# Performance work log

Hardware: AMD Instinct MI355X
Metric: run time of the kernel (lower is better)

## Reference

```python
import jax, jax.numpy as jnp
import numpy as np

N_NODES = 100000
N_EDGES = 1_600_000
N_ROIS = 400
HIDDEN = 128
N_GRAPHS = 512
OUT = 2


def setup_inputs() -> dict:
    key = jax.random.key(0)
    ks = jax.random.split(key, 7)
    x = jax.random.normal(ks[0], (N_NODES, N_ROIS), dtype=jnp.float32)
    edge_index = jax.random.randint(ks[1], (2, N_EDGES), 0, N_NODES, dtype=jnp.int32)
    # sorted graph-assignment vector; prepend arange so every graph id is non-empty
    rnd = jax.random.randint(ks[2], (N_NODES - N_GRAPHS,), 0, N_GRAPHS, dtype=jnp.int32)
    batch = jnp.sort(jnp.concatenate([jnp.arange(N_GRAPHS, dtype=jnp.int32), rnd]))
    W = jax.random.normal(ks[3], (N_ROIS, HIDDEN), dtype=jnp.float32) / np.float32(np.sqrt(N_ROIS))
    b = jnp.zeros((HIDDEN,), dtype=jnp.float32)
    lin_W = jax.random.normal(ks[4], (HIDDEN, OUT), dtype=jnp.float32) / np.float32(np.sqrt(HIDDEN))
    lin_b = jnp.zeros((OUT,), dtype=jnp.float32)
    return {"x": x, "edge_index": edge_index, "batch": batch,
            "W": W, "b": b, "lin_W": lin_W, "lin_b": lin_b}


def reference(x, edge_index, batch, W, b, lin_W, lin_b):
    N = x.shape[0]
    # GCNConv: add self-loops, symmetric normalization D^-1/2 (A+I) D^-1/2
    loops = jnp.arange(N, dtype=edge_index.dtype)
    row = jnp.concatenate([edge_index[0], loops])  # source
    col = jnp.concatenate([edge_index[1], loops])  # target
    deg = jax.ops.segment_sum(jnp.ones_like(col, dtype=x.dtype), col, num_segments=N)
    dinv = jnp.where(deg > 0, jax.lax.rsqrt(deg), 0.0)
    norm = dinv[row] * dinv[col]                   # [E+N]
    h = x @ W                                      # [N, H] transform before propagate
    msg = h[row] * norm[:, None]                   # [E+N, H]
    agg = jax.ops.segment_sum(msg, col, num_segments=N) + b
    act = jax.nn.relu(agg)                         # [N, H]
    # global max pool over graph ids (all segments guaranteed non-empty)
    pooled = jax.ops.segment_max(act, batch, num_segments=N_GRAPHS)  # [G, H]
    logits = pooled @ lin_W + lin_b                # [G, OUT]
    return logits, pooled
```

## Files before the change

kernel.cpp:

```cpp
#include <hip/hip_runtime.h>
#include <hip/hip_bf16.h>

#define N_NODES 100000
#define N_EDGES 1600000
#define N_ROIS  400
#define HID     128
#define N_GRAPHS 512
#define NOUT    2
#define NBUCK   391
#define BCAP    8192
#define ECH     4096
#define NPW     16
#define NBLK_BUCKET 391
#define NBLK_PREP   208
#define NBLK_GEMM   782

typedef __attribute__((ext_vector_type(8))) short short8;
typedef __attribute__((ext_vector_type(4))) float f32x4;

static __device__ __forceinline__ unsigned short f2bf(float f) {
  unsigned u = __float_as_uint(f);
  u += 0x7fffu + ((u >> 16) & 1u);
  return (unsigned short)(u >> 16);
}
static __device__ __forceinline__ float bf2f(unsigned short h) {
  return __uint_as_float(((unsigned)h) << 16);
}

static __device__ __forceinline__ void gload_lds16(const unsigned short* g, short* l) {
  __builtin_amdgcn_global_load_lds(
      (const __attribute__((address_space(1))) void*)g,
      (__attribute__((address_space(3))) void*)l, 16, 0, 0);
}

__global__ __launch_bounds__(256) void prep_bucket_k(
    const int* __restrict__ row, const int* __restrict__ col,
    int* __restrict__ bcnt, unsigned int* __restrict__ pairs,
    const float* __restrict__ W, unsigned short* __restrict__ Wf) {
  __shared__ int hist[NBUCK];
  __shared__ int lbase[NBUCK];
  __shared__ int adj[NBUCK];
  __shared__ unsigned int spk[ECH];
  __shared__ unsigned short sbk[ECH];
  __shared__ int sc[256];
  int t = threadIdx.x;
  if (blockIdx.x >= NBLK_BUCKET) {
    int idx = (blockIdx.x - NBLK_BUCKET) * 256 + t;
    if (idx < 13 * 8 * 64 * 8) {
      int u    = idx & 7;
      int lane = (idx >> 3) & 63;
      int nt   = (idx >> 9) & 7;
      int kk5  = idx >> 12;
      int n = nt * 16 + (lane & 15);
      int k = kk5 * 32 + (lane >> 4) * 8 + u;
      Wf[idx] = (k < N_ROIS) ? f2bf(W[k * HID + n]) : (unsigned short)0;
    }
    return;
  }
  for (int b = t; b < NBUCK; b += 256) hist[b] = 0;
  __syncthreads();
  int e0 = blockIdx.x * ECH;
  int mtot = min(ECH, N_EDGES - e0);
  unsigned int pk[16];
  int bk[16], rk[16];
#pragma unroll
  for (int i = 0; i < 16; ++i) {
    int e = e0 + t + i * 256;
    if (e < N_EDGES) {
      int r = row[e], c = col[e];
      bk[i] = c >> 8;
      pk[i] = ((unsigned)r << 8) | (unsigned)(c & 255);
      rk[i] = atomicAdd(&hist[bk[i]], 1);
    } else bk[i] = -1;
  }
  __syncthreads();
  int v0 = hist[t];
  sc[t] = v0;
  __syncthreads();
  for (int off = 1; off < 256; off <<= 1) {
    int v = (t >= off) ? sc[t - off] : 0;
    __syncthreads();
    sc[t] += v;
    __syncthreads();
  }
  lbase[t] = sc[t] - v0;
  int tot0 = sc[255];
  __syncthreads();
  int v1 = (t < NBUCK - 256) ? hist[256 + t] : 0;
  sc[t] = v1;
  __syncthreads();
  for (int off = 1; off < 256; off <<= 1) {
    int v = (t >= off) ? sc[t - off] : 0;
    __syncthreads();
    sc[t] += v;
    __syncthreads();
  }
  if (t < NBUCK - 256) lbase[256 + t] = tot0 + sc[t] - v1;
  __syncthreads();
#pragma unroll
  for (int i = 0; i < 16; ++i)
    if (bk[i] >= 0) {
      int pos = lbase[bk[i]] + rk[i];
      spk[pos] = pk[i];
      sbk[pos] = (unsigned short)bk[i];
    }
  for (int b = t; b < NBUCK; b += 256)
    adj[b] = (hist[b] > 0) ? atomicAdd(&bcnt[b], hist[b]) : 0;
  __syncthreads();
  for (int j = t; j < mtot; j += 256) {
    int b = sbk[j];
    int p = adj[b] + (j - lbase[b]);
    if (p < BCAP) pairs[(size_t)b * BCAP + p] = spk[j];
  }
}

__global__ __launch_bounds__(512, 4) void csr_gemm_k(
    const unsigned int* __restrict__ pairs, const int* __restrict__ bcnt,
    int* __restrict__ csr_row, int* __restrict__ offs, int* __restrict__ cnt,
    float* __restrict__ dinv,
    const float* __restrict__ x, const unsigned short* __restrict__ Wf,
    unsigned short* __restrict__ hp) {
  __shared__ __align__(16) union {
    struct {
      unsigned int ep[BCAP];
      int ssr[BCAP];
      int h[256]; int sc2[256]; int cur[256];
    } c;
    short Bs[28672];
  } u;
  int t = threadIdx.x;

  if (blockIdx.x < NBUCK) {
    bool act = t < 256;
    int b = blockIdx.x;
    int m = min(bcnt[b], BCAP);
    size_t base = (size_t)b * BCAP;
    for (int j = t; j < m; j += 512) u.c.ep[j] = pairs[base + j];
    if (act) u.c.h[t] = 0;
    __syncthreads();
    for (int j = t; j < m; j += 512) atomicAdd(&u.c.h[u.c.ep[j] & 255u], 1);
    __syncthreads();
    int myc = act ? u.c.h[t] : 0;
    int mycp = (myc + 3) & ~3;
    if (act) u.c.sc2[t] = mycp;
    __syncthreads();
    for (int off = 1; off < 256; off <<= 1) {
      int v = (act && t >= off) ? u.c.sc2[t - off] : 0;
      __syncthreads();
      if (act) u.c.sc2[t] += v;
      __syncthreads();
    }
    if (act) {
      int loff = u.c.sc2[t] - mycp;
      u.c.cur[t] = loff;
      int node = b * 256 + t;
      if (node < N_NODES) {
        cnt[node] = myc;
        offs[node] = (int)base + loff;
        dinv[node] = rsqrtf((float)(myc + 1));
      }
    }
    __syncthreads();
    for (int j = t; j < m; j += 512) {
      unsigned int e = u.c.ep[j];
      int pos = atomicAdd(&u.c.cur[e & 255u], 1);
      if (pos < BCAP) u.c.ssr[pos] = (int)(e >> 8);
    }
    __syncthreads();
    int tpad = u.c.sc2[255];
    if (tpad > BCAP) tpad = BCAP;
    for (int j = t; j < tpad; j += 512) csr_row[base + j] = u.c.ssr[j];
    return;
  }

  int lane = t & 63, wv = t >> 6;
  int mrow = lane & 15, kg = lane >> 4;
  int row0 = (blockIdx.x - NBUCK) * 128;
  int arow = row0 + wv * 16 + mrow;
  bool rowok = arow < N_NODES;
  const float* xp = x + (size_t)arow * N_ROIS;

  f32x4 acc[8];
#pragma unroll
  for (int i = 0; i < 8; ++i) acc[i] = (f32x4){0.f, 0.f, 0.f, 0.f};

#pragma unroll
  for (int c = 0; c < 7; ++c) {
    int ch = wv * 7 + c;
    gload_lds16(Wf + (size_t)ch * 512 + lane * 8, &u.Bs[ch * 512]);
  }
  asm volatile("s_waitcnt vmcnt(0)" ::: "memory");
  __syncthreads();

#pragma unroll
  for (int kf = 0; kf < 7; ++kf) {
    int k0 = kf * 32 + kg * 8;
    short8 a8;
    if (rowok && k0 + 8 <= N_ROIS) {
      float4 f0 = *(const float4*)(xp + k0);
      float4 f1 = *(const float4*)(xp + k0 + 4);
      a8[0] = (short)f2bf(f0.x); a8[1] = (short)f2bf(f0.y);
      a8[2] = (short)f2bf(f0.z); a8[3] = (short)f2bf(f0.w);
      a8[4] = (short)f2bf(f1.x); a8[5] = (short)f2bf(f1.y);
      a8[6] = (short)f2bf(f1.z); a8[7] = (short)f2bf(f1.w);
    } else {
#pragma unroll
      for (int v = 0; v < 8; ++v) {
        int k = k0 + v;
        float f = (rowok && k < N_ROIS) ? xp[k] : 0.f;
        a8[v] = (short)f2bf(f);
      }
    }
#pragma unroll
    for (int nt = 0; nt < 8; ++nt) {
      short8 bf = *(const short8*)&u.Bs[(kf * 8 + nt) * 512 + lane * 8];
      acc[nt] = __builtin_amdgcn_mfma_f32_16x16x32_bf16(a8, bf, acc[nt], 0, 0, 0);
    }
  }
  __syncthreads();

#pragma unroll
  for (int c = 0; c < 6; ++c) {
    int ch = wv * 6 + c;
    gload_lds16(Wf + (size_t)(56 + ch) * 512 + lane * 8, &u.Bs[ch * 512]);
  }
  asm volatile("s_waitcnt vmcnt(0)" ::: "memory");
  __syncthreads();

#pragma unroll
  for (int kf = 0; kf < 6; ++kf) {
    int k0 = (kf + 7) * 32 + kg * 8;
    short8 a8;
    if (rowok && k0 + 8 <= N_ROIS) {
      float4 f0 = *(const float4*)(xp + k0);
      float4 f1 = *(const float4*)(xp + k0 + 4);
      a8[0] = (short)f2bf(f0.x); a8[1] = (short)f2bf(f0.y);
      a8[2] = (short)f2bf(f0.z); a8[3] = (short)f2bf(f0.w);
      a8[4] = (short)f2bf(f1.x); a8[5] = (short)f2bf(f1.y);
      a8[6] = (short)f2bf(f1.z); a8[7] = (short)f2bf(f1.w);
    } else {
#pragma unroll
      for (int v = 0; v < 8; ++v) {
        int k = k0 + v;
        float f = (rowok && k < N_ROIS) ? xp[k] : 0.f;
        a8[v] = (short)f2bf(f);
      }
    }
#pragma unroll
    for (int nt = 0; nt < 8; ++nt) {
      short8 bf = *(const short8*)&u.Bs[(kf * 8 + nt) * 512 + lane * 8];
      acc[nt] = __builtin_amdgcn_mfma_f32_16x16x32_bf16(a8, bf, acc[nt], 0, 0, 0);
    }
  }

#pragma unroll
  for (int r = 0; r < 4; ++r) {
    int grow = row0 + wv * 16 + kg * 4 + r;
    if (grow < N_NODES) {
      unsigned short* op = hp + (size_t)grow * HID + mrow;
#pragma unroll
      for (int nt = 0; nt < 8; ++nt) op[nt * 16] = f2bf(acc[nt][r]);
    }
  }
}

static __device__ __forceinline__ void acc8s(float* a, uint4 u, float d) {
  a[0] = fmaf(d, bf2f((unsigned short)(u.x)), a[0]);
  a[1] = fmaf(d, bf2f((unsigned short)(u.x >> 16)), a[1]);
  a[2] = fmaf(d, bf2f((unsigned short)(u.y)), a[2]);
  a[3] = fmaf(d, bf2f((unsigned short)(u.y >> 16)), a[3]);
  a[4] = fmaf(d, bf2f((unsigned short)(u.z)), a[4]);
  a[5] = fmaf(d, bf2f((unsigned short)(u.z >> 16)), a[5]);
  a[6] = fmaf(d, bf2f((unsigned short)(u.w)), a[6]);
  a[7] = fmaf(d, bf2f((unsigned short)(u.w >> 16)), a[7]);
}

__global__ __launch_bounds__(256) void gather_k(
    const unsigned short* __restrict__ hp, const int* __restrict__ csr_row,
    const int* __restrict__ offs, const int* __restrict__ cnt,
    const float* __restrict__ dinv, const int* __restrict__ batch,
    const float* __restrict__ bias, unsigned int* __restrict__ pooled_bits) {
  int wave = (blockIdx.x * blockDim.x + threadIdx.x) >> 6;
  int lane = threadIdx.x & 63;
  int g  = lane >> 4;
  int cg = lane & 15;
  int n0 = wave * NPW;
  if (n0 >= N_NODES) return;
  int nend = min(n0 + NPW, N_NODES);
  float bv[8];
  {
    float4 b0 = *(const float4*)(bias + cg * 8);
    float4 b1 = *(const float4*)(bias + cg * 8 + 4);
    bv[0] = b0.x; bv[1] = b0.y; bv[2] = b0.z; bv[3] = b0.w;
    bv[4] = b1.x; bv[5] = b1.y; bv[6] = b1.z; bv[7] = b1.w;
  }
  float rm[8];
#pragma unroll
  for (int k = 0; k < 8; ++k) rm[k] = 0.f;
  int cur_g = batch[n0];

  for (int i = n0; i < nend; ++i) {
    int start = offs[i];
    int m = cnt[i];
    float di = dinv[i];
    float a[8];
#pragma unroll
    for (int k = 0; k < 8; ++k) a[k] = 0.f;
    if (g == 0) {
      uint4 u = *(const uint4*)(hp + (size_t)i * HID + cg * 8);
      acc8s(a, u, di);
    }
    for (int j = 0; j < m; j += 4) {
      int4 q = *(const int4*)(csr_row + start + j);
      int s = (g == 0) ? q.x : (g == 1) ? q.y : (g == 2) ? q.z : q.w;
      if (j + g < m) {
        float dv = dinv[s];
        uint4 u = *(const uint4*)(hp + (size_t)s * HID + cg * 8);
        acc8s(a, u, dv);
      }
    }
#pragma unroll
    for (int k = 0; k < 8; ++k) {
      a[k] += __shfl_xor(a[k], 16);
      a[k] += __shfl_xor(a[k], 32);
    }
    int gb = batch[i];
    if (gb != cur_g) {
      if (lane < 16) {
#pragma unroll
        for (int k = 0; k < 8; ++k)
          atomicMax(&pooled_bits[cur_g * HID + cg * 8 + k], __float_as_uint(rm[k]));
      }
#pragma unroll
      for (int k = 0; k < 8; ++k) rm[k] = 0.f;
      cur_g = gb;
    }
#pragma unroll
    for (int k = 0; k < 8; ++k)
      rm[k] = fmaxf(rm[k], fmaxf(fmaf(di, a[k], bv[k]), 0.f));
  }
  if (lane < 16) {
#pragma unroll
    for (int k = 0; k < 8; ++k)
      atomicMax(&pooled_bits[cur_g * HID + cg * 8 + k], __float_as_uint(rm[k]));
  }
}

__global__ void logits_k(const float* __restrict__ pooled, const float* __restrict__ lin_W,
                         const float* __restrict__ lin_b, float* __restrict__ out) {
  int t = blockIdx.x * blockDim.x + threadIdx.x;
  if (t < N_GRAPHS * NOUT) {
    int g = t >> 1, o = t & 1;
    float s = lin_b[o];
    const float* pg = pooled + g * HID;
#pragma unroll 8
    for (int k = 0; k < HID; ++k) s = fmaf(pg[k], lin_W[k * NOUT + o], s);
    out[t] = s;
  }
}

extern "C" void kernel_launch(void* const* d_in, const int* in_sizes, int n_in,
                              void* d_out, int out_size, void* d_ws, size_t ws_size,
                              hipStream_t stream) {
  (void)in_sizes; (void)n_in; (void)ws_size;
  const float* x     = (const float*)d_in[0];
  const int*   ei    = (const int*)d_in[1];
  const int*   row   = ei;
  const int*   col   = ei + N_EDGES;
  const int*   batch = (const int*)d_in[2];
  const float* W     = (const float*)d_in[3];
  const float* b     = (const float*)d_in[4];
  const float* lin_W = (const float*)d_in[5];
  const float* lin_b = (const float*)d_in[6];
  float* out = (float*)d_out;

  char* ws = (char*)d_ws;
  int*   bcnt    = (int*)(ws + 0);
  int*   offs    = (int*)(ws + 4096);
  int*   cnt     = (int*)(ws + 404096);
  float* dinv    = (float*)(ws + 804096);
  unsigned short* Wf = (unsigned short*)(ws + 1204096);
  int*   csr_row = (int*)(ws + 1310720);
  unsigned int* pairs = (unsigned int*)(ws + 14123008);
  unsigned short* hp  = (unsigned short*)(ws + 26935296);

  hipMemsetAsync(bcnt, 0, NBUCK * sizeof(int), stream);
  hipMemsetAsync(d_out, 0, (size_t)out_size * sizeof(float), stream);

  prep_bucket_k<<<NBLK_BUCKET + NBLK_PREP, 256, 0, stream>>>(row, col, bcnt, pairs, W, Wf);
  csr_gemm_k<<<NBUCK + NBLK_GEMM, 512, 0, stream>>>(
      pairs, bcnt, csr_row, offs, cnt, dinv, x, Wf, hp);
  {
    int waves = (N_NODES + NPW - 1) / NPW;
    int blocks = (waves * 64 + 255) / 256;
    gather_k<<<blocks, 256, 0, stream>>>(
        hp, csr_row, offs, cnt, dinv, batch, b,
        (unsigned int*)(out + N_GRAPHS * NOUT));
  }
  logits_k<<<(N_GRAPHS * NOUT + 255) / 256, 256, 0, stream>>>(
      out + N_GRAPHS * NOUT, lin_W, lin_b, out);
}
```

Baseline: 381.7 us.

## Drop LDS staging of W in GEMM, scatter CSR directly, fuse pooled zeroing

The GEMM blocks now read the pre-swizzled bf16 weight fragments straight from global memory (L2/L1 cached) instead of staging them through LDS with global_load_lds and barriers. The CSR bucket pass writes rows directly to global memory rather than through an LDS staging array, which shrinks the shared footprint. Pooled zeroing moves into the prep kernel, removing one memset, and f2bf switches to the HIP intrinsic. The smaller LDS union may raise occupancy, at the cost of more global/L1 traffic for W and uncoalesced CSR writes.

```diff
diff --git a/kernel.cpp b/kernel.cpp
--- a/kernel.cpp
+++ b/kernel.cpp
@@ -19,24 +19,20 @@
 typedef __attribute__((ext_vector_type(4))) float f32x4;
 
 static __device__ __forceinline__ unsigned short f2bf(float f) {
-  unsigned u = __float_as_uint(f);
-  u += 0x7fffu + ((u >> 16) & 1u);
-  return (unsigned short)(u >> 16);
+  __hip_bfloat16 h = __float2bfloat16(f);
+  unsigned short u;
+  __builtin_memcpy(&u, &h, 2);
+  return u;
 }
 static __device__ __forceinline__ float bf2f(unsigned short h) {
   return __uint_as_float(((unsigned)h) << 16);
-}
-
-static __device__ __forceinline__ void gload_lds16(const unsigned short* g, short* l) {
-  __builtin_amdgcn_global_load_lds(
-      (const __attribute__((address_space(1))) void*)g,
-      (__attribute__((address_space(3))) void*)l, 16, 0, 0);
 }
 
 __global__ __launch_bounds__(256) void prep_bucket_k(
     const int* __restrict__ row, const int* __restrict__ col,
     int* __restrict__ bcnt, unsigned int* __restrict__ pairs,
-    const float* __restrict__ W, unsigned short* __restrict__ Wf) {
+    const float* __restrict__ W, unsigned short* __restrict__ Wf,
+    float* __restrict__ pooled0) {
   __shared__ int hist[NBUCK];
   __shared__ int lbase[NBUCK];
   __shared__ int adj[NBUCK];
@@ -55,6 +51,11 @@
       int k = kk5 * 32 + (lane >> 4) * 8 + u;
       Wf[idx] = (k < N_ROIS) ? f2bf(W[k * HID + n]) : (unsigned short)0;
     }
+    int z = idx * 2;
+    if (z < N_GRAPHS * HID) {
+      float2 zz = {0.f, 0.f};
+      *(float2*)(pooled0 + z) = zz;
+    }
     return;
   }
   for (int b = t; b < NBUCK; b += 256) hist[b] = 0;
@@ -120,14 +121,10 @@
     float* __restrict__ dinv,
     const float* __restrict__ x, const unsigned short* __restrict__ Wf,
     unsigned short* __restrict__ hp) {
-  __shared__ __align__(16) union {
-    struct {
-      unsigned int ep[BCAP];
-      int ssr[BCAP];
-      int h[256]; int sc2[256]; int cur[256];
-    } c;
-    short Bs[28672];
-  } u;
+  __shared__ __align__(16) struct {
+    unsigned int ep[BCAP];
+    int h[256]; int sc2[256]; int cur[256];
+  } c;
   int t = threadIdx.x;
 
   if (blockIdx.x < NBUCK) {
@@ -135,24 +132,24 @@
     int b = blockIdx.x;
     int m = min(bcnt[b], BCAP);
     size_t base = (size_t)b * BCAP;
-    for (int j = t; j < m; j += 512) u.c.ep[j] = pairs[base + j];
-    if (act) u.c.h[t] = 0;
-    __syncthreads();
-    for (int j = t; j < m; j += 512) atomicAdd(&u.c.h[u.c.ep[j] & 255u], 1);
-    __syncthreads();
-    int myc = act ? u.c.h[t] : 0;
+    for (int j = t; j < m; j += 512) c.ep[j] = pairs[base + j];
+    if (act) c.h[t] = 0;
+    __syncthreads();
+    for (int j = t; j < m; j += 512) atomicAdd(&c.h[c.ep[j] & 255u], 1);
+    __syncthreads();
+    int myc = act ? c.h[t] : 0;
     int mycp = (myc + 3) & ~3;
-    if (act) u.c.sc2[t] = mycp;
+    if (act) c.sc2[t] = mycp;
     __syncthreads();
     for (int off = 1; off < 256; off <<= 1) {
-      int v = (act && t >= off) ? u.c.sc2[t - off] : 0;
+      int v = (act && t >= off) ? c.sc2[t - off] : 0;
       __syncthreads();
-      if (act) u.c.sc2[t] += v;
+      if (act) c.sc2[t] += v;
       __syncthreads();
     }
     if (act) {
-      int loff = u.c.sc2[t] - mycp;
-      u.c.cur[t] = loff;
+      int loff = c.sc2[t] - mycp;
+      c.cur[t] = loff;
       int node = b * 256 + t;
       if (node < N_NODES) {
         cnt[node] = myc;
@@ -162,14 +159,10 @@
     }
     __syncthreads();
     for (int j = t; j < m; j += 512) {
-      unsigned int e = u.c.ep[j];
-      int pos = atomicAdd(&u.c.cur[e & 255u], 1);
-      if (pos < BCAP) u.c.ssr[pos] = (int)(e >> 8);
-    }
-    __syncthreads();
-    int tpad = u.c.sc2[255];
-    if (tpad > BCAP) tpad = BCAP;
-    for (int j = t; j < tpad; j += 512) csr_row[base + j] = u.c.ssr[j];
+      unsigned int e = c.ep[j];
+      int pos = atomicAdd(&c.cur[e & 255u], 1);
+      if (pos < BCAP) csr_row[base + pos] = (int)(e >> 8);
+    }
     return;
   }
 
@@ -179,21 +172,14 @@
   int arow = row0 + wv * 16 + mrow;
   bool rowok = arow < N_NODES;
   const float* xp = x + (size_t)arow * N_ROIS;
+  const short8* wp = (const short8*)Wf + lane;
 
   f32x4 acc[8];
 #pragma unroll
   for (int i = 0; i < 8; ++i) acc[i] = (f32x4){0.f, 0.f, 0.f, 0.f};
 
 #pragma unroll
-  for (int c = 0; c < 7; ++c) {
-    int ch = wv * 7 + c;
-    gload_lds16(Wf + (size_t)ch * 512 + lane * 8, &u.Bs[ch * 512]);
-  }
-  asm volatile("s_waitcnt vmcnt(0)" ::: "memory");
-  __syncthreads();
-
-#pragma unroll
-  for (int kf = 0; kf < 7; ++kf) {
+  for (int kf = 0; kf < 13; ++kf) {
     int k0 = kf * 32 + kg * 8;
     short8 a8;
     if (rowok && k0 + 8 <= N_ROIS) {
@@ -213,42 +199,7 @@
     }
 #pragma unroll
     for (int nt = 0; nt < 8; ++nt) {
-      short8 bf = *(const short8*)&u.Bs[(kf * 8 + nt) * 512 + lane * 8];
-      acc[nt] = __builtin_amdgcn_mfma_f32_16x16x32_bf16(a8, bf, acc[nt], 0, 0, 0);
-    }
-  }
-  __syncthreads();
-
-#pragma unroll
-  for (int c = 0; c < 6; ++c) {
-    int ch = wv * 6 + c;
-    gload_lds16(Wf + (size_t)(56 + ch) * 512 + lane * 8, &u.Bs[ch * 512]);
-  }
-  asm volatile("s_waitcnt vmcnt(0)" ::: "memory");
-  __syncthreads();
-
-#pragma unroll
-  for (int kf = 0; kf < 6; ++kf) {
-    int k0 = (kf + 7) * 32 + kg * 8;
-    short8 a8;
-    if (rowok && k0 + 8 <= N_ROIS) {
-      float4 f0 = *(const float4*)(xp + k0);
-      float4 f1 = *(const float4*)(xp + k0 + 4);
-      a8[0] = (short)f2bf(f0.x); a8[1] = (short)f2bf(f0.y);
-      a8[2] = (short)f2bf(f0.z); a8[3] = (short)f2bf(f0.w);
-      a8[4] = (short)f2bf(f1.x); a8[5] = (short)f2bf(f1.y);
-      a8[6] = (short)f2bf(f1.z); a8[7] = (short)f2bf(f1.w);
-    } else {
-#pragma unroll
-      for (int v = 0; v < 8; ++v) {
-        int k = k0 + v;
-        float f = (rowok && k < N_ROIS) ? xp[k] : 0.f;
-        a8[v] = (short)f2bf(f);
-      }
-    }
-#pragma unroll
-    for (int nt = 0; nt < 8; ++nt) {
-      short8 bf = *(const short8*)&u.Bs[(kf * 8 + nt) * 512 + lane * 8];
+      short8 bf = wp[(kf * 8 + nt) * 64];
       acc[nt] = __builtin_amdgcn_mfma_f32_16x16x32_bf16(a8, bf, acc[nt], 0, 0, 0);
     }
   }
@@ -362,7 +313,7 @@
 extern "C" void kernel_launch(void* const* d_in, const int* in_sizes, int n_in,
                               void* d_out, int out_size, void* d_ws, size_t ws_size,
                               hipStream_t stream) {
-  (void)in_sizes; (void)n_in; (void)ws_size;
+  (void)in_sizes; (void)n_in; (void)ws_size; (void)out_size;
   const float* x     = (const float*)d_in[0];
   const int*   ei    = (const int*)d_in[1];
   const int*   row   = ei;
@@ -373,6 +324,7 @@
   const float* lin_W = (const float*)d_in[5];
   const float* lin_b = (const float*)d_in[6];
   float* out = (float*)d_out;
+  float* pooled0 = out + N_GRAPHS * NOUT;
 
   char* ws = (char*)d_ws;
   int*   bcnt    = (int*)(ws + 0);
@@ -385,9 +337,9 @@
   unsigned short* hp  = (unsigned short*)(ws + 26935296);
 
   hipMemsetAsync(bcnt, 0, NBUCK * sizeof(int), stream);
-  hipMemsetAsync(d_out, 0, (size_t)out_size * sizeof(float), stream);
-
-  prep_bucket_k<<<NBLK_BUCKET + NBLK_PREP, 256, 0, stream>>>(row, col, bcnt, pairs, W, Wf);
+
+  prep_bucket_k<<<NBLK_BUCKET + NBLK_PREP, 256, 0, stream>>>(
+      row, col, bcnt, pairs, W, Wf, pooled0);
   csr_gemm_k<<<NBUCK + NBLK_GEMM, 512, 0, stream>>>(
       pairs, bcnt, csr_row, offs, cnt, dinv, x, Wf, hp);
   {
@@ -395,8 +347,8 @@
     int blocks = (waves * 64 + 255) / 256;
     gather_k<<<blocks, 256, 0, stream>>>(
         hp, csr_row, offs, cnt, dinv, batch, b,
-        (unsigned int*)(out + N_GRAPHS * NOUT));
+        (unsigned int*)pooled0);
   }
   logits_k<<<(N_GRAPHS * NOUT + 255) / 256, 256, 0, stream>>>(
-      out + N_GRAPHS * NOUT, lin_W, lin_b, out);
-}
+      pooled0, lin_W, lin_b, out);
+}
```

Result: slower. 404.9 us (+6.1%).
